# Performance work log

Measured on AMD Instinct MI355X. Metric: run time of the kernel, lower is better.

Reference implementation:

```python
import jax, jax.numpy as jnp
import numpy as np

B, C, W, H = 32, 64, 96, 96
L = 32          # LSTM hidden size
OUT = 256       # conv output channels
EPS = 1e-5


def _lstm_dir(x, wih, whh, b):
    # x: [N, T, D]; wih: [4L, D]; whh: [4L, L]; b: [4L] (b_ih + b_hh)
    N, T, D = x.shape
    Lh = whh.shape[1]
    xg = jnp.einsum('ntd,gd->ntg', x, wih) + b  # precompute input projections

    def step(carry, xg_t):
        h, c = carry
        g = xg_t + h @ whh.T
        i, f, gg, o = jnp.split(g, 4, axis=-1)  # PyTorch gate order i,f,g,o
        i = jax.nn.sigmoid(i)
        f = jax.nn.sigmoid(f)
        gg = jnp.tanh(gg)
        o = jax.nn.sigmoid(o)
        c = f * c + i * gg
        h = o * jnp.tanh(c)
        return (h, c), h

    init = (jnp.zeros((N, Lh), x.dtype), jnp.zeros((N, Lh), x.dtype))
    _, hs = jax.lax.scan(step, init, jnp.swapaxes(xg, 0, 1))
    return jnp.swapaxes(hs, 0, 1)  # [N, T, L]


def _bilstm(x, wih_f, whh_f, bih_f, bhh_f, wih_b, whh_b, bih_b, bhh_b):
    hf = _lstm_dir(x, wih_f, whh_f, bih_f + bhh_f)
    hb = _lstm_dir(x[:, ::-1], wih_b, whh_b, bih_b + bhh_b)[:, ::-1]
    return jnp.concatenate([hf, hb], axis=-1)  # [N, T, 2L]


def setup_inputs() -> dict:
    key = jax.random.key(0)
    ks = jax.random.split(key, 24)
    s1 = 1.0 / np.sqrt(L)
    def u(k, shape):
        return jax.random.uniform(k, shape, jnp.float32, -s1, s1)
    inp = {'x': jax.random.normal(ks[0], (B, C, W, H), jnp.float32)}
    # vertical LSTM: input_size=C
    inp['v_wih_f'] = u(ks[1], (4 * L, C)); inp['v_whh_f'] = u(ks[2], (4 * L, L))
    inp['v_bih_f'] = u(ks[3], (4 * L,));  inp['v_bhh_f'] = u(ks[4], (4 * L,))
    inp['v_wih_b'] = u(ks[5], (4 * L, C)); inp['v_whh_b'] = u(ks[6], (4 * L, L))
    inp['v_bih_b'] = u(ks[7], (4 * L,));  inp['v_bhh_b'] = u(ks[8], (4 * L,))
    # horizontal LSTM: input_size=2L
    inp['h_wih_f'] = u(ks[9], (4 * L, 2 * L)); inp['h_whh_f'] = u(ks[10], (4 * L, L))
    inp['h_bih_f'] = u(ks[11], (4 * L,));      inp['h_bhh_f'] = u(ks[12], (4 * L,))
    inp['h_wih_b'] = u(ks[13], (4 * L, 2 * L)); inp['h_whh_b'] = u(ks[14], (4 * L, L))
    inp['h_bih_b'] = u(ks[15], (4 * L,));       inp['h_bhh_b'] = u(ks[16], (4 * L,))
    # 1x1 conv + BN
    inp['conv_w'] = jax.random.normal(ks[17], (OUT, 2 * L), jnp.float32) * 0.05
    inp['conv_b'] = jnp.zeros((OUT,), jnp.float32)
    inp['bn_g'] = jnp.ones((OUT,), jnp.float32)
    inp['bn_b'] = jnp.zeros((OUT,), jnp.float32)
    return inp


def reference(x, v_wih_f, v_whh_f, v_bih_f, v_bhh_f, v_wih_b, v_whh_b, v_bih_b, v_bhh_b,
              h_wih_f, h_whh_f, h_bih_f, h_bhh_f, h_wih_b, h_whh_b, h_bih_b, h_bhh_b,
              conv_w, conv_b, bn_g, bn_b):
    b, c, w, h = x.shape
    xt = jnp.transpose(x, (0, 3, 2, 1))  # [B, H, W, C] (torch transpose(1,3))
    # vertical pass: for each column w, LSTM over H -> batch all columns at once
    xv = jnp.transpose(xt, (0, 2, 1, 3)).reshape(b * w, h, c)  # [B*W, H, C]
    hv = _bilstm(xv, v_wih_f, v_whh_f, v_bih_f, v_bhh_f,
                 v_wih_b, v_whh_b, v_bih_b, v_bhh_b)            # [B*W, H, 2L]
    v = jnp.transpose(hv.reshape(b, w, h, 2 * L), (0, 2, 1, 3))  # [B, H, W, 2L]
    # horizontal pass: for each row h, LSTM over W -> batch all rows at once
    xh = v.reshape(b * h, w, 2 * L)
    hh = _bilstm(xh, h_wih_f, h_whh_f, h_bih_f, h_bhh_f,
                 h_wih_b, h_whh_b, h_bih_b, h_bhh_b).reshape(b, h, w, 2 * L)
    # stack(dim=3) then transpose(1,2) in torch == [B, 2L, W, H]
    y = jnp.transpose(hh, (0, 3, 2, 1))  # [B, 2L, W, H]
    # 1x1 conv
    y = jnp.einsum('bcwh,oc->bowh', y, conv_w) + conv_b[None, :, None, None]
    # BatchNorm2d (training mode: batch statistics, biased variance)
    mean = jnp.mean(y, axis=(0, 2, 3), keepdims=True)
    var = jnp.mean((y - mean) ** 2, axis=(0, 2, 3), keepdims=True)
    out = (y - mean) * jax.lax.rsqrt(var + EPS)
    out = out * bn_g[None, :, None, None] + bn_b[None, :, None, None]
    return out
```

## Files before the change

kernel.cpp:

```cpp
#include <hip/hip_runtime.h>
#include <stdint.h>

#define DI __device__ __forceinline__

constexpr int Bn = 32, Cc = 64, Wn = 96, Hn = 96, Ln = 32, NG = 128, OUTC = 256;
constexpr int SEQ = 96;
constexpr long long NPIX = (long long)Bn * Wn * Hn;
constexpr int GRAM_BLOCKS = 256;
constexpr int PIX_PER_BLOCK = (int)(NPIX / GRAM_BLOCKS);

typedef __attribute__((ext_vector_type(8))) short bf16x8;
typedef __attribute__((ext_vector_type(4))) float f32x4;

constexpr float LOG2E  = 1.44269504088896340736f;
constexpr float TWOL2E = 2.88539008177792681472f;

DI float exp2_(float x) { return __builtin_amdgcn_exp2f(x); }
DI float rcp_(float x)  { return __builtin_amdgcn_rcpf(x); }
DI float bf2f(unsigned short u) { return __uint_as_float(((unsigned)u) << 16); }
DI unsigned short f2bf(float f) {
    unsigned u = __float_as_uint(f);
    u += 0x7FFFu + ((u >> 16) & 1u);
    return (unsigned short)(u >> 16);
}

union U32x4 { unsigned u[4]; bf16x8 v; };

__global__ __launch_bounds__(256)
void transpose_x(const float* __restrict__ x, unsigned short* __restrict__ xT)
{
    __shared__ alignas(16) unsigned char xs[96 * 128];
    const int tid = threadIdx.x;
    const int b = blockIdx.x / 96, q = blockIdx.x % 96;
    for (int i = tid; i < 1536; i += 256) {
        int c = i / 24, h4 = i - c * 24;
        float4 v = *(const float4*)(x + (((size_t)b * 64 + c) * 96 + q) * 96 + 4 * h4);
        float vv[4] = {v.x, v.y, v.z, v.w};
#pragma unroll
        for (int j = 0; j < 4; ++j) {
            int h = 4 * h4 + j;
            *(unsigned short*)(xs + h * 128 + ((c * 2) ^ ((h & 7) << 4))) = f2bf(vv[j]);
        }
    }
    __syncthreads();
    unsigned short* ob = xT + (size_t)blockIdx.x * 6144;
    for (int i = tid; i < 768; i += 256) {
        int row = i >> 3, k8 = i & 7;
        bf16x8 p = *(const bf16x8*)(xs + row * 128 + ((k8 * 16) ^ ((row & 7) << 4)));
        *(bf16x8*)(ob + (size_t)i * 8) = p;
    }
}

#define FLOAD(XA, XB, STI)                                                     \
    if ((STI) < 96) {                                                          \
        const int tl_ = dir ? 95 - (STI) : (STI);                              \
        XA = *(const bf16x8*)(xTb + (size_t)tl_ * 64);                         \
        XB = *(const bf16x8*)(xTb + (size_t)tl_ * 64 + 32);                    \
    }

#define PPROJ(XA, XB)                                                          \
    _Pragma("unroll")                                                          \
    for (int tt = 0; tt < 8; ++tt) {                                           \
        f32x4 tp_ = __builtin_amdgcn_mfma_f32_16x16x32_bf16(ax0[tt], XA, bc[tt], 0, 0, 0); \
        xac[tt] = __builtin_amdgcn_mfma_f32_16x16x32_bf16(ax1[tt], XB, tp_, 0, 0, 0);      \
    }

#define RSTEP(STI)                                                             \
    {                                                                          \
        const int t_ = dir ? 95 - (STI) : (STI);                               \
        U32x4 hu;                                                              \
        {                                                                      \
            int a0 = __shfl((int)pk0x, srcL0), a1 = __shfl((int)pk0y, srcL0);  \
            int a2 = __shfl((int)pk0x, srcL1), a3 = __shfl((int)pk0y, srcL1);  \
            int b0 = __shfl((int)pk1x, srcL0), b1 = __shfl((int)pk1y, srcL0);  \
            int b2 = __shfl((int)pk1x, srcL1), b3 = __shfl((int)pk1y, srcL1);  \
            hu.u[0] = sp ? (unsigned)b0 : (unsigned)a0;                        \
            hu.u[1] = sp ? (unsigned)b1 : (unsigned)a1;                        \
            hu.u[2] = sp ? (unsigned)b2 : (unsigned)a2;                        \
            hu.u[3] = sp ? (unsigned)b3 : (unsigned)a3;                        \
        }                                                                      \
        f32x4 ac_[8];                                                          \
        _Pragma("unroll")                                                      \
        for (int tt = 0; tt < 8; ++tt)                                         \
            ac_[tt] = __builtin_amdgcn_mfma_f32_16x16x32_bf16(ah[tt], hu.v, xac[tt], 0, 0, 0); \
        _Pragma("unroll")                                                      \
        for (int s = 0; s < 2; ++s) {                                          \
            unsigned short hs[4];                                              \
            _Pragma("unroll")                                                  \
            for (int j = 0; j < 4; ++j) {                                      \
                const float iv = rcp_(1.f + exp2_(-ac_[0 + s][j]));            \
                const float fv = rcp_(1.f + exp2_(-ac_[2 + s][j]));            \
                const float gr = rcp_(1.f + exp2_(-ac_[4 + s][j]));            \
                const float gv = fmaf(2.f, gr, -1.f);                          \
                const float ov = rcp_(1.f + exp2_(-ac_[6 + s][j]));            \
                cc[s][j] = fmaf(fv, cc[s][j], iv * gv);                        \
                const float r_ = rcp_(exp2_(cc[s][j] * TWOL2E) + 1.f);         \
                const float t2 = -2.f * ov;                                    \
                hs[j] = f2bf(fmaf(t2, r_, ov));                                \
            }                                                                  \
            const unsigned dlo = ((unsigned)hs[1] << 16) | hs[0];              \
            const unsigned dhi = ((unsigned)hs[3] << 16) | hs[2];              \
            if (s == 0) { pk0x = dlo; pk0y = dhi; } else { pk1x = dlo; pk1y = dhi; } \
            ushort4 hp; hp.x = hs[0]; hp.y = hs[1]; hp.z = hs[2]; hp.w = hs[3];\
            const int cbase = dir * 32 + s * 16 + rg * 4;                      \
            const size_t oidx = VERT                                           \
                ? ((((size_t)b * 96 + t_) * 96 + q) * 64 + cbase)              \
                : ((((size_t)b * 96 + q) * 96 + t_) * 64 + cbase);             \
            *(ushort4*)(outU + oidx) = hp;                                     \
        }                                                                      \
    }

template<int VERT>
__global__ __launch_bounds__(64, 1)
void lstm_fused(const unsigned short* __restrict__ xT,
                const float* __restrict__ wih_f, const float* __restrict__ whh_f,
                const float* __restrict__ bih_f, const float* __restrict__ bhh_f,
                const float* __restrict__ wih_b, const float* __restrict__ whh_b,
                const float* __restrict__ bih_b, const float* __restrict__ bhh_b,
                unsigned short* __restrict__ outU)
{
    const int lane = threadIdx.x;
    const int dir = blockIdx.x & 1, group = blockIdx.x >> 1;
    const int n_ = lane & 15, rg = lane >> 4;
    const int chain = group * 16 + n_;
    const int b = group / 6;
    const int q = (group % 6) * 16 + n_;

    const float* wih = dir ? wih_b : wih_f;
    const float* whh = dir ? whh_b : whh_f;
    const float* bih = dir ? bih_b : bih_f;
    const float* bhh = dir ? bhh_b : bhh_f;

    bf16x8 ah[8], ax0[8], ax1[8];
    f32x4 bc[8];
#pragma unroll
    for (int tt = 0; tt < 8; ++tt) {
        const float sc = (tt == 4 || tt == 5) ? TWOL2E : LOG2E;
        const float* sh = whh + (size_t)(tt * 16 + n_) * 32 + rg * 8;
        const float* sx = wih + (size_t)(tt * 16 + n_) * 64 + rg * 8;
        float4 h0 = *(const float4*)sh, h1 = *(const float4*)(sh + 4);
        float4 x0 = *(const float4*)sx, x1 = *(const float4*)(sx + 4);
        float4 x2 = *(const float4*)(sx + 32), x3 = *(const float4*)(sx + 36);
        ah[tt][0] = (short)f2bf(sc * h0.x); ah[tt][1] = (short)f2bf(sc * h0.y);
        ah[tt][2] = (short)f2bf(sc * h0.z); ah[tt][3] = (short)f2bf(sc * h0.w);
        ah[tt][4] = (short)f2bf(sc * h1.x); ah[tt][5] = (short)f2bf(sc * h1.y);
        ah[tt][6] = (short)f2bf(sc * h1.z); ah[tt][7] = (short)f2bf(sc * h1.w);
        ax0[tt][0] = (short)f2bf(sc * x0.x); ax0[tt][1] = (short)f2bf(sc * x0.y);
        ax0[tt][2] = (short)f2bf(sc * x0.z); ax0[tt][3] = (short)f2bf(sc * x0.w);
        ax0[tt][4] = (short)f2bf(sc * x1.x); ax0[tt][5] = (short)f2bf(sc * x1.y);
        ax0[tt][6] = (short)f2bf(sc * x1.z); ax0[tt][7] = (short)f2bf(sc * x1.w);
        ax1[tt][0] = (short)f2bf(sc * x2.x); ax1[tt][1] = (short)f2bf(sc * x2.y);
        ax1[tt][2] = (short)f2bf(sc * x2.z); ax1[tt][3] = (short)f2bf(sc * x2.w);
        ax1[tt][4] = (short)f2bf(sc * x3.x); ax1[tt][5] = (short)f2bf(sc * x3.y);
        ax1[tt][6] = (short)f2bf(sc * x3.z); ax1[tt][7] = (short)f2bf(sc * x3.w);
#pragma unroll
        for (int j = 0; j < 4; ++j) {
            const int g = tt * 16 + rg * 4 + j;
            bc[tt][j] = sc * (bih[g] + bhh[g]);
        }
    }

    const int sp = rg >> 1;
    const int srcL0 = ((rg & 1) << 1) * 16 + n_;
    const int srcL1 = srcL0 + 16;

    const unsigned short* xTb = xT + (size_t)chain * 6144 + rg * 8;

    unsigned pk0x = 0, pk0y = 0, pk1x = 0, pk1y = 0;
    float cc[2][4];
#pragma unroll
    for (int s = 0; s < 2; ++s)
#pragma unroll
        for (int j = 0; j < 4; ++j) cc[s][j] = 0.f;

    f32x4 xac[8];
    bf16x8 xa0, xb0, xa1, xb1, xa2, xb2;
    FLOAD(xa0, xb0, 0)
    FLOAD(xa1, xb1, 1)
    PPROJ(xa0, xb0)

    for (int st = 0; st < 96; st += 3) {
        FLOAD(xa2, xb2, st + 2)
        RSTEP(st)
        PPROJ(xa1, xb1)
        FLOAD(xa0, xb0, st + 3)
        RSTEP(st + 1)
        PPROJ(xa2, xb2)
        FLOAD(xa1, xb1, st + 4)
        RSTEP(st + 2)
        PPROJ(xa0, xb0)
    }
}

__global__ __launch_bounds__(256)
void gram_partial(const unsigned short* __restrict__ hh, float* __restrict__ part)
{
    __shared__ float xs[64][64];
    __shared__ float red[4160];
    const int tid = threadIdx.x;
    for (int e = tid; e < 4160; e += 256) red[e] = 0.0f;
    const int lane = tid & 63, wv = tid >> 6;
    const int li = lane >> 3, lj = lane & 7;
    float acc[8][8]; float macc[8];
#pragma unroll
    for (int i = 0; i < 8; ++i) {
        macc[i] = 0.f;
#pragma unroll
        for (int j = 0; j < 8; ++j) acc[i][j] = 0.f;
    }
    const size_t pix0 = (size_t)blockIdx.x * PIX_PER_BLOCK;
    for (int tile = 0; tile < PIX_PER_BLOCK / 64; ++tile) {
        __syncthreads();
        const unsigned short* src = hh + (pix0 + tile * 64) * 64;
#pragma unroll
        for (int r = 0; r < 4; ++r) {
            int idx4 = tid + 256 * r;
            ushort4 v = ((const ushort4*)src)[idx4];
            int fi = idx4 * 4; int px = fi >> 6; int c = fi & 63;
            xs[px][c] = bf2f(v.x); xs[px][c + 1] = bf2f(v.y);
            xs[px][c + 2] = bf2f(v.z); xs[px][c + 3] = bf2f(v.w);
        }
        __syncthreads();
        for (int p = wv * 16; p < wv * 16 + 16; ++p) {
            float4 ra = *(const float4*)&xs[p][8 * li];
            float4 rb = *(const float4*)&xs[p][8 * li + 4];
            float4 ca = *(const float4*)&xs[p][8 * lj];
            float4 cb = *(const float4*)&xs[p][8 * lj + 4];
            float r[8] = {ra.x, ra.y, ra.z, ra.w, rb.x, rb.y, rb.z, rb.w};
            float cl[8] = {ca.x, ca.y, ca.z, ca.w, cb.x, cb.y, cb.z, cb.w};
#pragma unroll
            for (int i = 0; i < 8; ++i) {
#pragma unroll
                for (int j = 0; j < 8; ++j) acc[i][j] = fmaf(r[i], cl[j], acc[i][j]);
            }
            if (lj == 0) {
#pragma unroll
                for (int i = 0; i < 8; ++i) macc[i] += r[i];
            }
        }
    }
    __syncthreads();
#pragma unroll
    for (int i = 0; i < 8; ++i)
#pragma unroll
        for (int j = 0; j < 8; ++j)
            atomicAdd(&red[(8 * li + i) * 64 + 8 * lj + j], acc[i][j]);
    if (lj == 0)
        for (int i = 0; i < 8; ++i) atomicAdd(&red[4096 + 8 * li + i], macc[i]);
    __syncthreads();
    for (int e = tid; e < 4160; e += 256) part[(size_t)blockIdx.x * 4160 + e] = red[e];
}

__global__ void gram_reduce(const float* __restrict__ part, float* __restrict__ M)
{
    int e = blockIdx.x * 256 + threadIdx.x;
    if (e >= 4160) return;
    double s = 0.0;
    for (int p = 0; p < GRAM_BLOCKS; ++p) s += (double)part[(size_t)p * 4160 + e];
    M[e] = (float)s;
}

__global__ __launch_bounds__(256)
void stats_kernel(const float* __restrict__ M, const float* __restrict__ cw,
                  const float* __restrict__ cb, const float* __restrict__ bg,
                  const float* __restrict__ bb,
                  float* __restrict__ Aout, float* __restrict__ Bout)
{
    __shared__ float Ml[4160];
    const int tid = threadIdx.x;
    for (int e = tid; e < 4160; e += 256) Ml[e] = M[e];
    __syncthreads();
    float wr[64];
#pragma unroll
    for (int c = 0; c < 64; ++c) wr[c] = bf2f(f2bf(cw[tid * 64 + c]));
    float s1 = 0.f;
#pragma unroll
    for (int c = 0; c < 64; ++c) s1 = fmaf(wr[c], Ml[4096 + c], s1);
    float s2 = 0.f;
    for (int c = 0; c < 64; ++c) {
        const float* Mr = &Ml[c * 64];
        float t = 0.f;
#pragma unroll
        for (int d = 0; d < 64; ++d) t = fmaf(wr[d], Mr[d], t);
        s2 = fmaf(wr[c], t, s2);
    }
    const double invN = 1.0 / (double)NPIX;
    double cbo = (double)cb[tid];
    double mu = (double)s1 * invN + cbo;
    double ey2 = (double)s2 * invN + 2.0 * cbo * ((double)s1 * invN) + cbo * cbo;
    double var = ey2 - mu * mu;
    double A = (double)bg[tid] / sqrt(var + 1e-5);
    Aout[tid] = (float)A;
    Bout[tid] = (float)((double)bb[tid] + A * (cbo - mu));
}

__global__ __launch_bounds__(512, 2)
void conv_bn_kernel(const unsigned short* __restrict__ hh, const float* __restrict__ cw,
                    const float* __restrict__ Aarr, const float* __restrict__ Barr,
                    float* __restrict__ out)
{
    __shared__ alignas(16) unsigned char UsB[96 * 128];
    __shared__ alignas(16) unsigned char WtB[256 * 128];

    const int tid = threadIdx.x;
    const int b = blockIdx.x / 96, w = blockIdx.x % 96;

    for (int i4 = tid; i4 < 4096; i4 += 512) {
        int wrow = i4 >> 4, k4 = i4 & 15;
        float4 v = *(const float4*)(cw + (size_t)wrow * 64 + k4 * 4);
        ushort4 p; p.x = f2bf(v.x); p.y = f2bf(v.y); p.z = f2bf(v.z); p.w = f2bf(v.w);
        *(ushort4*)(WtB + wrow * 128 + ((k4 * 8) ^ ((wrow & 7) << 4))) = p;
    }
    for (int i = tid; i < 1536; i += 512) {
        int row = i >> 4, k4 = i & 15;
        ushort4 p = *(const ushort4*)(hh + (((size_t)b * 96 + row) * 96 + w) * 64 + k4 * 4);
        *(ushort4*)(UsB + row * 128 + ((k4 * 8) ^ ((row & 7) << 4))) = p;
    }
    __syncthreads();

    const int wv = tid >> 6, lane = tid & 63;
    const int mbase = (wv >> 2) * 48, nbase = (wv & 3) * 64;
    const int lrow = lane & 15, lk = (lane >> 4) * 8;

    f32x4 acc[3][4];
#pragma unroll
    for (int m = 0; m < 3; ++m)
#pragma unroll
        for (int n = 0; n < 4; ++n)
            acc[m][n] = (f32x4){0.f, 0.f, 0.f, 0.f};

#pragma unroll
    for (int ks = 0; ks < 2; ++ks) {
        const int kb = (ks * 32 + lk) * 2;
        bf16x8 am[3], bn[4];
#pragma unroll
        for (int m = 0; m < 3; ++m) {
            int row = mbase + m * 16 + lrow;
            am[m] = *(const bf16x8*)(UsB + row * 128 + (kb ^ ((row & 7) << 4)));
        }
#pragma unroll
        for (int n = 0; n < 4; ++n) {
            int o = nbase + n * 16 + lrow;
            bn[n] = *(const bf16x8*)(WtB + o * 128 + (kb ^ ((o & 7) << 4)));
        }
#pragma unroll
        for (int m = 0; m < 3; ++m)
#pragma unroll
            for (int n = 0; n < 4; ++n)
                acc[m][n] = __builtin_amdgcn_mfma_f32_16x16x32_bf16(am[m], bn[n], acc[m][n], 0, 0, 0);
    }

    const int hbase0 = (lane >> 4) * 4;
#pragma unroll
    for (int n = 0; n < 4; ++n) {
        const int o = nbase + n * 16 + lrow;
        const float Ao = Aarr[o], Bo = Barr[o];
        float* obase = out + (((size_t)b * 256 + o) * 96 + w) * 96;
#pragma unroll
        for (int m = 0; m < 3; ++m) {
            const int h0 = mbase + m * 16 + hbase0;
            float4 res;
            res.x = fmaf(Ao, acc[m][n][0], Bo);
            res.y = fmaf(Ao, acc[m][n][1], Bo);
            res.z = fmaf(Ao, acc[m][n][2], Bo);
            res.w = fmaf(Ao, acc[m][n][3], Bo);
            *(float4*)(obase + h0) = res;
        }
    }
}

extern "C" void kernel_launch(void* const* d_in, const int* in_sizes, int n_in,
                              void* d_out, int out_size, void* d_ws, size_t ws_size,
                              hipStream_t stream)
{
    const float* x       = (const float*)d_in[0];
    const float* v_wih_f = (const float*)d_in[1];
    const float* v_whh_f = (const float*)d_in[2];
    const float* v_bih_f = (const float*)d_in[3];
    const float* v_bhh_f = (const float*)d_in[4];
    const float* v_wih_b = (const float*)d_in[5];
    const float* v_whh_b = (const float*)d_in[6];
    const float* v_bih_b = (const float*)d_in[7];
    const float* v_bhh_b = (const float*)d_in[8];
    const float* h_wih_f = (const float*)d_in[9];
    const float* h_whh_f = (const float*)d_in[10];
    const float* h_bih_f = (const float*)d_in[11];
    const float* h_bhh_f = (const float*)d_in[12];
    const float* h_wih_b = (const float*)d_in[13];
    const float* h_whh_b = (const float*)d_in[14];
    const float* h_bih_b = (const float*)d_in[15];
    const float* h_bhh_b = (const float*)d_in[16];
    const float* conv_w  = (const float*)d_in[17];
    const float* conv_b  = (const float*)d_in[18];
    const float* bn_g    = (const float*)d_in[19];
    const float* bn_b    = (const float*)d_in[20];
    float* out = (float*)d_out;

    const size_t v_elems = (size_t)Bn * Hn * Wn * 64;
    unsigned short* v_buf = (unsigned short*)(out + (size_t)out_size) - v_elems;
    unsigned short* xT = (unsigned short*)d_out;
    float* part = (float*)((char*)d_out + (64u << 20));

    unsigned short* hh = (unsigned short*)d_ws;
    char* wsb = (char*)d_ws;
    float* M    = (float*)(wsb + 37748736);
    float* Aarr = M + 4160;
    float* Barr = Aarr + 256;

    transpose_x<<<3072, 256, 0, stream>>>(x, xT);
    lstm_fused<1><<<384, 64, 0, stream>>>(xT, v_wih_f, v_whh_f, v_bih_f, v_bhh_f,
                                          v_wih_b, v_whh_b, v_bih_b, v_bhh_b, v_buf);
    lstm_fused<0><<<384, 64, 0, stream>>>(v_buf, h_wih_f, h_whh_f, h_bih_f, h_bhh_f,
                                          h_wih_b, h_whh_b, h_bih_b, h_bhh_b, hh);
    gram_partial<<<GRAM_BLOCKS, 256, 0, stream>>>(hh, part);
    gram_reduce<<<17, 256, 0, stream>>>(part, M);
    stats_kernel<<<1, 256, 0, stream>>>(M, conv_w, conv_b, bn_g, bn_b, Aarr, Barr);
    conv_bn_kernel<<<3072, 512, 0, stream>>>(hh, conv_w, Aarr, Barr, out);
}
```

Before: 414.6 us.

## Use MFMA for Gram partials, strength-reduce LSTM output indexing, nontemporal final stores

The Gram-matrix partial kernel moves from scalar FP32 outer products with LDS atomics to bf16 MFMA over a transposed, padded, double-buffered LDS tile. Column sums are now accumulated during the load, and results are written straight to the partial buffer without an atomic reduction. The LSTM output address is now advanced by a pointer increment each step instead of recomputing the full index. The final normalized output uses nontemporal stores to avoid polluting the cache. These are independent tweaks across three kernels, and the LSTM recurrence is likely the dominant cost.

```diff
diff --git a/kernel.cpp b/kernel.cpp
--- a/kernel.cpp
+++ b/kernel.cpp
@@ -67,7 +67,6 @@
 
 #define RSTEP(STI)                                                             \
     {                                                                          \
-        const int t_ = dir ? 95 - (STI) : (STI);                               \
         U32x4 hu;                                                              \
         {                                                                      \
             int a0 = __shfl((int)pk0x, srcL0), a1 = __shfl((int)pk0y, srcL0);  \
@@ -102,12 +101,9 @@
             const unsigned dhi = ((unsigned)hs[3] << 16) | hs[2];              \
             if (s == 0) { pk0x = dlo; pk0y = dhi; } else { pk1x = dlo; pk1y = dhi; } \
             ushort4 hp; hp.x = hs[0]; hp.y = hs[1]; hp.z = hs[2]; hp.w = hs[3];\
-            const int cbase = dir * 32 + s * 16 + rg * 4;                      \
-            const size_t oidx = VERT                                           \
-                ? ((((size_t)b * 96 + t_) * 96 + q) * 64 + cbase)              \
-                : ((((size_t)b * 96 + q) * 96 + t_) * 64 + cbase);             \
-            *(ushort4*)(outU + oidx) = hp;                                     \
+            *(ushort4*)(optr + s * 16) = hp;                                   \
         }                                                                      \
+        optr += odelta;                                                        \
     }
 
 template<int VERT>
@@ -166,6 +162,12 @@
 
     const unsigned short* xTb = xT + (size_t)chain * 6144 + rg * 8;
 
+    const int t0 = dir ? 95 : 0;
+    const size_t o0 = VERT ? ((((size_t)b * 96 + t0) * 96 + q) * 64)
+                           : ((((size_t)b * 96 + q) * 96 + t0) * 64);
+    unsigned short* optr = outU + o0 + dir * 32 + rg * 4;
+    const ptrdiff_t odelta = (ptrdiff_t)(dir ? -1 : 1) * (VERT ? 6144 : 64);
+
     unsigned pk0x = 0, pk0y = 0, pk1x = 0, pk1y = 0;
     float cc[2][4];
 #pragma unroll
@@ -192,63 +194,64 @@
     }
 }
 
-__global__ __launch_bounds__(256)
+__global__ __launch_bounds__(256, 2)
 void gram_partial(const unsigned short* __restrict__ hh, float* __restrict__ part)
 {
-    __shared__ float xs[64][64];
-    __shared__ float red[4160];
+    __shared__ alignas(16) unsigned char xsT[2][64 * 144];
+    __shared__ float sumb[16][64];
+
     const int tid = threadIdx.x;
-    for (int e = tid; e < 4160; e += 256) red[e] = 0.0f;
-    const int lane = tid & 63, wv = tid >> 6;
-    const int li = lane >> 3, lj = lane & 7;
-    float acc[8][8]; float macc[8];
-#pragma unroll
-    for (int i = 0; i < 8; ++i) {
-        macc[i] = 0.f;
-#pragma unroll
-        for (int j = 0; j < 8; ++j) acc[i][j] = 0.f;
-    }
+    const int wv = tid >> 6, lane = tid & 63;
+    const int lrow = lane & 15, lkg = lane >> 4;
+    const int cq = tid & 15, pr = tid >> 4;
+
+    float csum[4] = {0.f, 0.f, 0.f, 0.f};
+    f32x4 acc[4];
+#pragma unroll
+    for (int n = 0; n < 4; ++n) acc[n] = (f32x4){0.f, 0.f, 0.f, 0.f};
+
     const size_t pix0 = (size_t)blockIdx.x * PIX_PER_BLOCK;
+
     for (int tile = 0; tile < PIX_PER_BLOCK / 64; ++tile) {
+        unsigned char* Xb = xsT[tile & 1];
+#pragma unroll
+        for (int r = 0; r < 4; ++r) {
+            const int p = pr + r * 16;
+            ushort4 v = *(const ushort4*)(hh + (pix0 + (size_t)tile * 64 + p) * 64 + cq * 4);
+            csum[0] += bf2f(v.x); csum[1] += bf2f(v.y);
+            csum[2] += bf2f(v.z); csum[3] += bf2f(v.w);
+            *(unsigned short*)(Xb + (cq * 4 + 0) * 144 + p * 2) = v.x;
+            *(unsigned short*)(Xb + (cq * 4 + 1) * 144 + p * 2) = v.y;
+            *(unsigned short*)(Xb + (cq * 4 + 2) * 144 + p * 2) = v.z;
+            *(unsigned short*)(Xb + (cq * 4 + 3) * 144 + p * 2) = v.w;
+        }
         __syncthreads();
-        const unsigned short* src = hh + (pix0 + tile * 64) * 64;
-#pragma unroll
-        for (int r = 0; r < 4; ++r) {
-            int idx4 = tid + 256 * r;
-            ushort4 v = ((const ushort4*)src)[idx4];
-            int fi = idx4 * 4; int px = fi >> 6; int c = fi & 63;
-            xs[px][c] = bf2f(v.x); xs[px][c + 1] = bf2f(v.y);
-            xs[px][c + 2] = bf2f(v.z); xs[px][c + 3] = bf2f(v.w);
-        }
-        __syncthreads();
-        for (int p = wv * 16; p < wv * 16 + 16; ++p) {
-            float4 ra = *(const float4*)&xs[p][8 * li];
-            float4 rb = *(const float4*)&xs[p][8 * li + 4];
-            float4 ca = *(const float4*)&xs[p][8 * lj];
-            float4 cb = *(const float4*)&xs[p][8 * lj + 4];
-            float r[8] = {ra.x, ra.y, ra.z, ra.w, rb.x, rb.y, rb.z, rb.w};
-            float cl[8] = {ca.x, ca.y, ca.z, ca.w, cb.x, cb.y, cb.z, cb.w};
-#pragma unroll
-            for (int i = 0; i < 8; ++i) {
-#pragma unroll
-                for (int j = 0; j < 8; ++j) acc[i][j] = fmaf(r[i], cl[j], acc[i][j]);
+#pragma unroll
+        for (int kc = 0; kc < 2; ++kc) {
+            const int kb = (kc * 32 + lkg * 8) * 2;
+            bf16x8 af = *(const bf16x8*)(Xb + (wv * 16 + lrow) * 144 + kb);
+#pragma unroll
+            for (int n = 0; n < 4; ++n) {
+                bf16x8 bf_ = *(const bf16x8*)(Xb + (n * 16 + lrow) * 144 + kb);
+                acc[n] = __builtin_amdgcn_mfma_f32_16x16x32_bf16(af, bf_, acc[n], 0, 0, 0);
             }
-            if (lj == 0) {
-#pragma unroll
-                for (int i = 0; i < 8; ++i) macc[i] += r[i];
-            }
-        }
-    }
+        }
+    }
+
+    *(float4*)&sumb[pr][cq * 4] = (float4){csum[0], csum[1], csum[2], csum[3]};
     __syncthreads();
-#pragma unroll
-    for (int i = 0; i < 8; ++i)
-#pragma unroll
-        for (int j = 0; j < 8; ++j)
-            atomicAdd(&red[(8 * li + i) * 64 + 8 * lj + j], acc[i][j]);
-    if (lj == 0)
-        for (int i = 0; i < 8; ++i) atomicAdd(&red[4096 + 8 * li + i], macc[i]);
-    __syncthreads();
-    for (int e = tid; e < 4160; e += 256) part[(size_t)blockIdx.x * 4160 + e] = red[e];
+    float* pb = part + (size_t)blockIdx.x * 4160;
+    if (tid < 64) {
+        float s = 0.f;
+#pragma unroll
+        for (int r = 0; r < 16; ++r) s += sumb[r][tid];
+        pb[4096 + tid] = s;
+    }
+#pragma unroll
+    for (int n = 0; n < 4; ++n)
+#pragma unroll
+        for (int r = 0; r < 4; ++r)
+            pb[(wv * 16 + lkg * 4 + r) * 64 + n * 16 + lrow] = acc[n][r];
 }
 
 __global__ void gram_reduce(const float* __restrict__ part, float* __restrict__ M)
@@ -359,12 +362,12 @@
 #pragma unroll
         for (int m = 0; m < 3; ++m) {
             const int h0 = mbase + m * 16 + hbase0;
-            float4 res;
-            res.x = fmaf(Ao, acc[m][n][0], Bo);
-            res.y = fmaf(Ao, acc[m][n][1], Bo);
-            res.z = fmaf(Ao, acc[m][n][2], Bo);
-            res.w = fmaf(Ao, acc[m][n][3], Bo);
-            *(float4*)(obase + h0) = res;
+            f32x4 res;
+            res[0] = fmaf(Ao, acc[m][n][0], Bo);
+            res[1] = fmaf(Ao, acc[m][n][1], Bo);
+            res[2] = fmaf(Ao, acc[m][n][2], Bo);
+            res[3] = fmaf(Ao, acc[m][n][3], Bo);
+            __builtin_nontemporal_store(res, (f32x4*)(obase + h0));
         }
     }
 }
```

Measured after the change: 347.3 us. 1.19x faster.
